# Optimization experiments

Measured on AMD Instinct MI355X. Metric: run time of the kernel, lower is better.

## Reference

```python
import jax, jax.numpy as jnp
import numpy as np

N = 262144   # cohort size (k_n)
M = 8192     # number of ordinal anchor indices (len(Hj))


def setup_inputs() -> dict:
    key = jax.random.key(0)
    k1, k2, k3, k4, k5 = jax.random.split(key, 5)
    time = jax.random.uniform(k1, (N,), dtype=jnp.float32) * 1000.0
    event = (jax.random.uniform(k2, (N,), dtype=jnp.float32) < 0.3).astype(jnp.float32)
    y_true0 = jnp.stack([time, event], axis=1)          # [N,2] (time, event)
    y_true1 = y_true0                                    # second head labels (unused by loss)
    y_pred0 = jax.random.normal(k3, (N, 1), dtype=jnp.float32) * 0.1  # xbeta head 0
    y_pred1 = jax.random.normal(k4, (N, 1), dtype=jnp.float32) * 0.1  # xbeta head 1
    Hj = jnp.sort(jax.random.randint(k5, (M,), 0, N, dtype=jnp.int32))  # static event indices into sorted order
    log_vars = jnp.zeros((2, 1), dtype=jnp.float32)      # layer weights log_var0, log_var1
    return {"y_true0": y_true0, "y_true1": y_true1, "y_pred0": y_pred0,
            "y_pred1": y_pred1, "Hj": Hj, "log_vars": log_vars}


def reference(y_true0, y_true1, y_pred0, y_pred1, Hj, log_vars):
    n = y_true0.shape[0]
    # top_k with k = n == full descending sort by time
    _, order = jax.lax.top_k(y_true0[:, 0], n)

    # ---- neg_log_pl (Cox negative partial log-likelihood, per-sample vector) ----
    xbeta = y_pred0[order, 0]                 # [N] sorted by descending time
    event = y_true0[order, 1]                 # [N]
    denom = jnp.cumsum(jnp.exp(xbeta))        # risk-set cumulative sum
    lossA = -(event * (xbeta - jnp.log(denom)))  # [N]

    # ---- ordinal_loss0 (pairwise ranking over event indices Hj in sorted order) ----
    # intended math: for each j, for ii >= j: cost += 1 - exp(xbeta[Hj[j]] - xbeta[Hj[ii]])
    xb = y_pred1[order, 0]                    # [N] sorted
    xh = xb[Hj]                               # [M]
    m = Hj.shape[0]
    rec = 1.0 - jnp.exp(xh[:, None] - xh[None, :])   # [M,M] rec[j,ii]
    mask = jnp.triu(jnp.ones((m, m), dtype=bool))    # ii >= j
    cost2 = jnp.sum(jnp.where(mask, rec, 0.0))

    # ---- multi_loss combination with learned log variances ----
    lv0 = log_vars[0, 0]
    lv1 = log_vars[1, 0]
    precision1 = jnp.clip(jnp.exp(-lv1), 0.0, 1.0)
    loss = jnp.sum(lossA + lv0) + (precision1 * cost2 + lv1)
    return loss


if __name__ == "__main__":
    out = reference(**setup_inputs())
    print(out)
```

## Files before the change

kernel.cpp:

```cpp
#include <hip/hip_runtime.h>
#include <math.h>


#define BSHIFT 12
#define NBUCK (1 << 19)
#define NREP 4
#define BLK 256
#define NC1 32

#define STORE_U32(p, v) __hip_atomic_store((p), (v), __ATOMIC_RELAXED, __HIP_MEMORY_SCOPE_AGENT)
#define STORE_F32(p, v) __hip_atomic_store((p), (v), __ATOMIC_RELAXED, __HIP_MEMORY_SCOPE_AGENT)
#define STORE_U64(p, v) __hip_atomic_store((unsigned long long*)(p), (v), __ATOMIC_RELAXED, __HIP_MEMORY_SCOPE_AGENT)

template <int GRID>
__device__ __forceinline__ void gbar(unsigned* bar, unsigned gv) {
  __syncthreads();
  if (threadIdx.x == 0) {
    constexpr unsigned BPC = GRID / NC1;
    const unsigned grp = blockIdx.x & (NC1 - 1);
    unsigned a = __hip_atomic_fetch_add(bar + grp * 16, 1u,
                                        __ATOMIC_RELAXED, __HIP_MEMORY_SCOPE_AGENT);
    if (a == gv * BPC - 1u) {
      unsigned b = __hip_atomic_fetch_add(bar + 512, 1u,
                                          __ATOMIC_RELAXED, __HIP_MEMORY_SCOPE_AGENT);
      if (b == gv * NC1 - 1u) {
        #pragma unroll
        for (int i = 0; i < NC1; ++i)
          STORE_U32(bar + 544 + i * 16, gv);
      }
    }
    int guard = 0;
    while (__hip_atomic_load(bar + 544 + grp * 16, __ATOMIC_RELAXED,
                             __HIP_MEMORY_SCOPE_AGENT) < gv) {
      __builtin_amdgcn_s_sleep(8);
      if (++guard > 8000000) break;
    }
  }
  __syncthreads();
}

template <int GRID>
__global__ void __launch_bounds__(BLK, 4)
k_fused(const float2* __restrict__ yt0, const float* __restrict__ yp0,
        const float* __restrict__ yp1, const int* __restrict__ Hj,
        const float* __restrict__ lv, int n, int m,
        unsigned* __restrict__ bar,
        unsigned* __restrict__ count, unsigned* __restrict__ E,
        unsigned* __restrict__ bTot, uint2* __restrict__ skey2,
        unsigned* __restrict__ sidx, float* __restrict__ preS,
        float* __restrict__ seTot, float* __restrict__ xh,
        double* __restrict__ accum, float* __restrict__ out)
{
  constexpr int TOT = GRID * BLK;
  constexpr int BPB = NBUCK / GRID;
  constexpr int BPT = BPB / BLK;
  const int t = threadIdx.x;
  const int g = blockIdx.x;
  const int gtid = g * BLK + t;

  __shared__ unsigned su[BLK];
  __shared__ float    sf[BLK];
  __shared__ float    pb[512];
  __shared__ double   sd[BLK];
  __shared__ float    wt[4];

  const int r = g & (NREP - 1);
  unsigned keyR[2]; float seR[2]; unsigned seqR[2]; unsigned evR[2];
  #pragma unroll
  for (int el = 0; el < 2; ++el) {
    int i = gtid + el * TOT;
    keyR[el] = 0u; seR[el] = 0.f; seqR[el] = 0u; evR[el] = 0u;
    if (i < n) {
      float2 te = yt0[i];
      unsigned key = __float_as_uint(te.x);
      keyR[el] = key;
      evR[el] = (te.y != 0.f) ? 0x80000000u : 0u;
      seR[el] = expf(yp0[i]);
      seqR[el] = atomicAdd(&count[(size_t)(key >> BSHIFT) * NREP + r], 1u);
    }
  }
  gbar<GRID>(bar, 1);

  unsigned incl[BPT]; unsigned thrBase;
  {
    unsigned run = 0u;
    #pragma unroll
    for (int k = 0; k < BPT; ++k) {
      int b = g * BPB + t * BPT + k;
      uint4 c = ((const uint4*)count)[b];
      run += c.x + c.y + c.z + c.w;
      incl[k] = run;
    }
    su[t] = run;
    __syncthreads();
    for (int off2 = 1; off2 < BLK; off2 <<= 1) {
      unsigned v = (t >= off2) ? su[t - off2] : 0u;
      __syncthreads();
      su[t] += v;
      __syncthreads();
    }
    thrBase = (t > 0) ? su[t - 1] : 0u;
    if (t == BLK - 1) STORE_U32(&bTot[g], su[t]);
  }
  gbar<GRID>(bar, 2);

  {
    unsigned part = 0u;
    for (int j = t; j < g; j += BLK) part += bTot[j];
    su[t] = part;
    __syncthreads();
    for (int s = BLK / 2; s > 0; s >>= 1) { if (t < s) su[t] += su[t + s]; __syncthreads(); }
    unsigned bBase = su[0];
    __syncthreads();
    unsigned e0 = bBase + thrBase;
    int ebase = g * BPB + t * BPT;
    if constexpr (BPT == 2) {
      unsigned long long w = ((unsigned long long)(e0 + incl[0]) << 32) | e0;
      STORE_U64(&E[ebase], w);
    } else {
      unsigned long long w0 = ((unsigned long long)(e0 + incl[0]) << 32) | e0;
      unsigned long long w1 = ((unsigned long long)(e0 + incl[2]) << 32) | (e0 + incl[1]);
      STORE_U64(&E[ebase], w0);
      STORE_U64(&E[ebase + 2], w1);
    }
  }
  gbar<GRID>(bar, 3);

  #pragma unroll
  for (int el = 0; el < 2; ++el) {
    int i = gtid + el * TOT;
    if (i < n) {
      unsigned key = keyR[el];
      unsigned b = key >> BSHIFT;
      uint4 c = ((const uint4*)count)[b];
      unsigned cnt = c.x + c.y + c.z + c.w;
      unsigned offr = 0u;
      if (r > 0) offr += c.x;
      if (r > 1) offr += c.y;
      if (r > 2) offr += c.z;
      unsigned start = (unsigned)n - E[b] - cnt;
      unsigned pos = start + offr + seqR[el];
      unsigned long long v =
          ((unsigned long long)__float_as_uint(seR[el]) << 32) | key;
      STORE_U64(&skey2[pos], v);
      STORE_U32(&sidx[pos], (unsigned)i | evR[el]);
    }
  }
  gbar<GRID>(bar, 4);

  if (g < 512) {
    int base = g * (2 * BLK);
    int p0 = base + 2 * t, p1 = p0 + 1;
    float e0 = (p0 < n) ? __uint_as_float(skey2[p0].y) : 0.f;
    float e1 = (p1 < n) ? __uint_as_float(skey2[p1].y) : 0.f;
    float pairv = e0 + e1;
    sf[t] = pairv;
    __syncthreads();
    for (int off2 = 1; off2 < BLK; off2 <<= 1) {
      float v = (t >= off2) ? sf[t - off2] : 0.f;
      __syncthreads();
      sf[t] += v;
      __syncthreads();
    }
    float ex = sf[t] - pairv;
    if (p0 < n) STORE_F32(&preS[p0], ex + e0);
    if (p1 < n) STORE_F32(&preS[p1], ex + e0 + e1);
    if (t == BLK - 1) STORE_F32(&seTot[g], sf[t]);
  }
  gbar<GRID>(bar, 5);

  {
    float a0 = seTot[2 * t];
    float a1 = seTot[2 * t + 1];
    float pairv = a0 + a1;
    sf[t] = pairv;
    __syncthreads();
    for (int off2 = 1; off2 < BLK; off2 <<= 1) {
      float v = (t >= off2) ? sf[t - off2] : 0.f;
      __syncthreads();
      sf[t] += v;
      __syncthreads();
    }
    pb[2 * t]     = sf[t] - a1;
    pb[2 * t + 1] = sf[t];
    __syncthreads();

    double contrib = 0.0;
    #pragma unroll
    for (int el = 0; el < 2; ++el) {
      int p = gtid + el * TOT;
      if (p >= n) continue;
      uint2 kv = skey2[p];
      unsigned key = kv.x;
      float e = __uint_as_float(kv.y);
      unsigned sidv = sidx[p];
      unsigned idx = sidv & 0x7FFFFFFFu;
      bool evb = (sidv >> 31) != 0u;
      unsigned b = key >> BSHIFT;
      uint4 c4 = ((const uint4*)count)[b];
      unsigned cnt = c4.x + c4.y + c4.z + c4.w;
      unsigned end = (unsigned)n - E[b];
      unsigned start = end - cnt;
      if (end > (unsigned)n) end = (unsigned)n;
      if (start > end) start = end;
      float wsum = 0.f;
      unsigned wcnt = 0u;
      unsigned q = start;
      while (q + 8 <= end) {
        uint2 v[8];
        #pragma unroll
        for (int k = 0; k < 8; ++k) v[k] = skey2[q + k];
        #pragma unroll
        for (int k = 0; k < 8; ++k) {
          if (v[k].x > key) { wsum += __uint_as_float(v[k].y); wcnt++; }
          else if (v[k].x == key && (sidx[q + k] & 0x7FFFFFFFu) < idx) {
            wsum += __uint_as_float(v[k].y); wcnt++;
          }
        }
        q += 8;
      }
      for (; q < end; ++q) {
        uint2 v = skey2[q];
        if (v.x > key) { wsum += __uint_as_float(v.y); wcnt++; }
        else if (v.x == key && (sidx[q] & 0x7FFFFFFFu) < idx) {
          wsum += __uint_as_float(v.y); wcnt++;
        }
      }
      unsigned sb = start >> 9;
      float cross = ((sb > 0) ? pb[sb - 1] : 0.f)
                  + ((start & 511u) ? preS[start - 1] : 0.f);
      float denom = cross + wsum + e;
      int rank = (int)(start + wcnt);
      if (evb) contrib += (double)logf(denom / e);
      int lo = 0, hi = m;
      while (lo < hi) { int mid = (lo + hi) >> 1; if (Hj[mid] < rank) lo = mid + 1; else hi = mid; }
      if (lo < m && Hj[lo] == rank) {
        float xb1 = yp1[idx];
        for (int j = lo; j < m && Hj[j] == rank; ++j) STORE_F32(&xh[j], xb1);
      }
    }
    sd[t] = contrib;
    __syncthreads();
    for (int s = 128; s > 0; s >>= 1) { if (t < s) sd[t] += sd[t + s]; __syncthreads(); }
    if (t == 0) atomicAdd(accum, sd[0]);
  }
  gbar<GRID>(bar, 6);

  if (g != 0) return;
  {
    int lane = t & 63;
    int w = t >> 6;
    double acc = 0.0;
    float carry = 0.f;
    int passes = (m + 2047) / 2048;
    for (int pss = passes - 1; pss >= 0; --pss) {
      int base = pss * 2048 + t * 8;
      float x[8], eb[8];
      float c = 0.f;
      #pragma unroll
      for (int k = 0; k < 8; ++k) {
        int j = base + k;
        x[k] = (j < m) ? xh[j] : 0.f;
        eb[k] = (j < m) ? expf(-x[k]) : 0.f;
        c += eb[k];
      }
      float s = c;
      #pragma unroll
      for (int d = 1; d < 64; d <<= 1) {
        float o = __shfl_down(s, d, 64);
        if (lane + d < 64) s += o;
      }
      float wtot = __shfl(s, 0, 64);
      if (lane == 0) wt[w] = wtot;
      __syncthreads();
      float after = 0.f, ptot = 0.f;
      #pragma unroll
      for (int w2 = 0; w2 < 4; ++w2) { ptot += wt[w2]; if (w2 > w) after += wt[w2]; }
      float S = (s - c) + after + carry;
      #pragma unroll
      for (int k = 7; k >= 0; --k) {
        int j = base + k;
        S += eb[k];
        if (j < m) acc += (double)(expf(x[k]) * S);
      }
      __syncthreads();
      carry += ptot;
    }
    sd[t] = acc;
    __syncthreads();
    for (int s2 = 128; s2 > 0; s2 >>= 1) { if (t < s2) sd[t] += sd[t + s2]; __syncthreads(); }
    if (t == 0) {
      double T = (double)m * (double)(m + 1) * 0.5;
      double cost2 = T - sd[0];
      float lv0 = lv[0], lv1 = lv[1];
      float prec1 = fminf(expf(-lv1), 1.0f);
      double loss = *accum + (double)n * (double)lv0 + (double)prec1 * cost2 + (double)lv1;
      out[0] = (float)loss;
    }
  }
}

extern "C" void kernel_launch(void* const* d_in, const int* in_sizes, int n_in,
                              void* d_out, int out_size, void* d_ws, size_t ws_size,
                              hipStream_t stream) {
  (void)n_in; (void)out_size;
  const float2* yt0 = (const float2*)d_in[0];
  const float*  yp0 = (const float*)d_in[2];
  const float*  yp1 = (const float*)d_in[3];
  const int*    Hj  = (const int*)d_in[4];
  const float*  lv  = (const float*)d_in[5];
  int n = in_sizes[0] / 2;
  int m = in_sizes[4];

  char* ws = (char*)d_ws;
  unsigned* bar   = (unsigned*)ws;
  double*   accum = (double*)(ws + 6144);
  size_t off = 8192;
  auto alloc = [&](size_t bytes) -> void* {
    void* p = ws + off;
    off += (bytes + 255) & ~(size_t)255;
    return p;
  };
  unsigned* count = (unsigned*)alloc((size_t)NBUCK * NREP * 4);
  unsigned* E     = (unsigned*)alloc((size_t)NBUCK * 4);
  unsigned* bTot  = (unsigned*)alloc(1024 * 4);
  uint2*    skey2 = (uint2*)alloc((size_t)n * 8);
  unsigned* sidx  = (unsigned*)alloc((size_t)n * 4);
  float*    preS  = (float*)alloc((size_t)n * 4);
  float*    seTot = (float*)alloc(1024 * 4);
  float*    xh    = (float*)alloc((size_t)m * 4);
  if (off > ws_size) return;

  hipMemsetAsync(ws, 0, 8192 + (size_t)NBUCK * NREP * 4, stream);

  k_fused<1024><<<dim3(1024), dim3(BLK), 0, stream>>>(
      yt0, yp0, yp1, Hj, lv, n, m, bar, count, E, bTot, skey2, sidx,
      preS, seTot, xh, accum, (float*)d_out);
}
```

Measured before the change: 138.1 us.

## Fold per-bucket exp sums into histogram atomics and drop the global prefix-scan stages

```diff
diff --git a/kernel.cpp b/kernel.cpp
--- a/kernel.cpp
+++ b/kernel.cpp
@@ -4,9 +4,9 @@
 
 #define BSHIFT 12
 #define NBUCK (1 << 19)
-#define NREP 4
 #define BLK 256
 #define NC1 32
+#define M40 ((1ull << 40) - 1)
 
 #define STORE_U32(p, v) __hip_atomic_store((p), (v), __ATOMIC_RELAXED, __HIP_MEMORY_SCOPE_AGENT)
 #define STORE_F32(p, v) __hip_atomic_store((p), (v), __ATOMIC_RELAXED, __HIP_MEMORY_SCOPE_AGENT)
@@ -32,8 +32,8 @@
     int guard = 0;
     while (__hip_atomic_load(bar + 544 + grp * 16, __ATOMIC_RELAXED,
                              __HIP_MEMORY_SCOPE_AGENT) < gv) {
-      __builtin_amdgcn_s_sleep(8);
-      if (++guard > 8000000) break;
+      __builtin_amdgcn_s_sleep(1);
+      if (++guard > 2000000) break;
     }
   }
   __syncthreads();
@@ -45,10 +45,10 @@
         const float* __restrict__ yp1, const int* __restrict__ Hj,
         const float* __restrict__ lv, int n, int m,
         unsigned* __restrict__ bar,
-        unsigned* __restrict__ count, unsigned* __restrict__ E,
-        unsigned* __restrict__ bTot, uint2* __restrict__ skey2,
-        unsigned* __restrict__ sidx, float* __restrict__ preS,
-        float* __restrict__ seTot, float* __restrict__ xh,
+        unsigned long long* __restrict__ rec, unsigned* __restrict__ bitmap,
+        uint4* __restrict__ Epack, unsigned* __restrict__ bTot,
+        float* __restrict__ fTot, uint2* __restrict__ skey2,
+        unsigned* __restrict__ sidx, float* __restrict__ xh,
         double* __restrict__ accum, float* __restrict__ out)
 {
   constexpr int TOT = GRID * BLK;
@@ -59,12 +59,10 @@
   const int gtid = g * BLK + t;
 
   __shared__ unsigned su[BLK];
-  __shared__ float    sf[BLK];
-  __shared__ float    pb[512];
+  __shared__ float    sff[BLK];
   __shared__ double   sd[BLK];
   __shared__ float    wt[4];
 
-  const int r = g & (NREP - 1);
   unsigned keyR[2]; float seR[2]; unsigned seqR[2]; unsigned evR[2];
   #pragma unroll
   for (int el = 0; el < 2; ++el) {
@@ -75,53 +73,70 @@
       unsigned key = __float_as_uint(te.x);
       keyR[el] = key;
       evR[el] = (te.y != 0.f) ? 0x80000000u : 0u;
-      seR[el] = expf(yp0[i]);
-      seqR[el] = atomicAdd(&count[(size_t)(key >> BSHIFT) * NREP + r], 1u);
-    }
+      float e = expf(yp0[i]);
+      seR[el] = e;
+      unsigned long long qe = (unsigned long long)(e * 16777216.0f + 0.5f);
+      if (qe > (1ull << 32)) qe = (1ull << 32);
+      unsigned long long ret =
+          atomicAdd(&rec[key >> BSHIFT], (1ull << 40) | qe);
+      seqR[el] = (unsigned)(ret >> 40);
+    }
+  }
+  for (int j = gtid; j < m; j += TOT) {
+    int h = Hj[j];
+    atomicOr(&bitmap[h >> 5], 1u << (h & 31));
   }
   gbar<GRID>(bar, 1);
 
-  unsigned incl[BPT]; unsigned thrBase;
+  unsigned cK[BPT]; float fK[BPT];
+  unsigned thrC; float thrF;
   {
-    unsigned run = 0u;
+    unsigned runc = 0u; float runf = 0.f;
     #pragma unroll
     for (int k = 0; k < BPT; ++k) {
-      int b = g * BPB + t * BPT + k;
-      uint4 c = ((const uint4*)count)[b];
-      run += c.x + c.y + c.z + c.w;
-      incl[k] = run;
-    }
-    su[t] = run;
+      int b = NBUCK - 1 - (g * BPB + t * BPT + k);
+      unsigned long long v = rec[b];
+      cK[k] = (unsigned)(v >> 40);
+      fK[k] = (float)((double)(v & M40) * (1.0 / 16777216.0));
+      runc += cK[k]; runf += fK[k];
+    }
+    su[t] = runc; sff[t] = runf;
     __syncthreads();
     for (int off2 = 1; off2 < BLK; off2 <<= 1) {
-      unsigned v = (t >= off2) ? su[t - off2] : 0u;
-      __syncthreads();
-      su[t] += v;
-      __syncthreads();
-    }
-    thrBase = (t > 0) ? su[t - 1] : 0u;
-    if (t == BLK - 1) STORE_U32(&bTot[g], su[t]);
+      unsigned uc = (t >= off2) ? su[t - off2] : 0u;
+      float    uf = (t >= off2) ? sff[t - off2] : 0.f;
+      __syncthreads();
+      su[t] += uc; sff[t] += uf;
+      __syncthreads();
+    }
+    thrC = (t > 0) ? su[t - 1] : 0u;
+    thrF = (t > 0) ? sff[t - 1] : 0.f;
+    if (t == BLK - 1) { STORE_U32(&bTot[g], su[t]); STORE_F32(&fTot[g], sff[t]); }
   }
   gbar<GRID>(bar, 2);
 
   {
-    unsigned part = 0u;
-    for (int j = t; j < g; j += BLK) part += bTot[j];
-    su[t] = part;
-    __syncthreads();
-    for (int s = BLK / 2; s > 0; s >>= 1) { if (t < s) su[t] += su[t + s]; __syncthreads(); }
-    unsigned bBase = su[0];
-    __syncthreads();
-    unsigned e0 = bBase + thrBase;
-    int ebase = g * BPB + t * BPT;
-    if constexpr (BPT == 2) {
-      unsigned long long w = ((unsigned long long)(e0 + incl[0]) << 32) | e0;
-      STORE_U64(&E[ebase], w);
-    } else {
-      unsigned long long w0 = ((unsigned long long)(e0 + incl[0]) << 32) | e0;
-      unsigned long long w1 = ((unsigned long long)(e0 + incl[2]) << 32) | (e0 + incl[1]);
-      STORE_U64(&E[ebase], w0);
-      STORE_U64(&E[ebase + 2], w1);
+    unsigned partC = 0u; float partF = 0.f;
+    for (int j = t; j < g; j += BLK) { partC += bTot[j]; partF += fTot[j]; }
+    su[t] = partC; sff[t] = partF;
+    __syncthreads();
+    for (int s = BLK / 2; s > 0; s >>= 1) {
+      if (t < s) { su[t] += su[t + s]; sff[t] += sff[t + s]; }
+      __syncthreads();
+    }
+    unsigned baseC = su[0]; float baseF = sff[0];
+    __syncthreads();
+    unsigned preC = 0u; float preF = 0.f;
+    #pragma unroll
+    for (int k = 0; k < BPT; ++k) {
+      int b = NBUCK - 1 - (g * BPB + t * BPT + k);
+      unsigned sfxC = baseC + thrC + preC;
+      float    sfxF = baseF + thrF + preF;
+      unsigned long long w =
+          ((unsigned long long)__float_as_uint(sfxF) << 32) | sfxC;
+      STORE_U64(&Epack[b].x, w);
+      STORE_U32(&Epack[b].z, cK[k]);
+      preC += cK[k]; preF += fK[k];
     }
   }
   gbar<GRID>(bar, 3);
@@ -132,14 +147,8 @@
     if (i < n) {
       unsigned key = keyR[el];
       unsigned b = key >> BSHIFT;
-      uint4 c = ((const uint4*)count)[b];
-      unsigned cnt = c.x + c.y + c.z + c.w;
-      unsigned offr = 0u;
-      if (r > 0) offr += c.x;
-      if (r > 1) offr += c.y;
-      if (r > 2) offr += c.z;
-      unsigned start = (unsigned)n - E[b] - cnt;
-      unsigned pos = start + offr + seqR[el];
+      unsigned start = Epack[b].x;
+      unsigned pos = start + seqR[el];
       unsigned long long v =
           ((unsigned long long)__float_as_uint(seR[el]) << 32) | key;
       STORE_U64(&skey2[pos], v);
@@ -148,59 +157,21 @@
   }
   gbar<GRID>(bar, 4);
 
-  if (g < 512) {
-    int base = g * (2 * BLK);
-    int p0 = base + 2 * t, p1 = p0 + 1;
-    float e0 = (p0 < n) ? __uint_as_float(skey2[p0].y) : 0.f;
-    float e1 = (p1 < n) ? __uint_as_float(skey2[p1].y) : 0.f;
-    float pairv = e0 + e1;
-    sf[t] = pairv;
-    __syncthreads();
-    for (int off2 = 1; off2 < BLK; off2 <<= 1) {
-      float v = (t >= off2) ? sf[t - off2] : 0.f;
-      __syncthreads();
-      sf[t] += v;
-      __syncthreads();
-    }
-    float ex = sf[t] - pairv;
-    if (p0 < n) STORE_F32(&preS[p0], ex + e0);
-    if (p1 < n) STORE_F32(&preS[p1], ex + e0 + e1);
-    if (t == BLK - 1) STORE_F32(&seTot[g], sf[t]);
-  }
-  gbar<GRID>(bar, 5);
-
   {
-    float a0 = seTot[2 * t];
-    float a1 = seTot[2 * t + 1];
-    float pairv = a0 + a1;
-    sf[t] = pairv;
-    __syncthreads();
-    for (int off2 = 1; off2 < BLK; off2 <<= 1) {
-      float v = (t >= off2) ? sf[t - off2] : 0.f;
-      __syncthreads();
-      sf[t] += v;
-      __syncthreads();
-    }
-    pb[2 * t]     = sf[t] - a1;
-    pb[2 * t + 1] = sf[t];
-    __syncthreads();
-
     double contrib = 0.0;
     #pragma unroll
     for (int el = 0; el < 2; ++el) {
-      int p = gtid + el * TOT;
-      if (p >= n) continue;
-      uint2 kv = skey2[p];
-      unsigned key = kv.x;
-      float e = __uint_as_float(kv.y);
-      unsigned sidv = sidx[p];
-      unsigned idx = sidv & 0x7FFFFFFFu;
-      bool evb = (sidv >> 31) != 0u;
+      int i = gtid + el * TOT;
+      if (i >= n) continue;
+      unsigned key = keyR[el];
+      float e = seR[el];
+      unsigned idx = (unsigned)i;
+      bool evb = evR[el] != 0u;
       unsigned b = key >> BSHIFT;
-      uint4 c4 = ((const uint4*)count)[b];
-      unsigned cnt = c4.x + c4.y + c4.z + c4.w;
-      unsigned end = (unsigned)n - E[b];
-      unsigned start = end - cnt;
+      uint4 ep = Epack[b];
+      unsigned start = ep.x;
+      float cross = __uint_as_float(ep.y);
+      unsigned end = start + ep.z;
       if (end > (unsigned)n) end = (unsigned)n;
       if (start > end) start = end;
       float wsum = 0.f;
@@ -226,17 +197,16 @@
           wsum += __uint_as_float(v.y); wcnt++;
         }
       }
-      unsigned sb = start >> 9;
-      float cross = ((sb > 0) ? pb[sb - 1] : 0.f)
-                  + ((start & 511u) ? preS[start - 1] : 0.f);
       float denom = cross + wsum + e;
       int rank = (int)(start + wcnt);
       if (evb) contrib += (double)logf(denom / e);
-      int lo = 0, hi = m;
-      while (lo < hi) { int mid = (lo + hi) >> 1; if (Hj[mid] < rank) lo = mid + 1; else hi = mid; }
-      if (lo < m && Hj[lo] == rank) {
-        float xb1 = yp1[idx];
-        for (int j = lo; j < m && Hj[j] == rank; ++j) STORE_F32(&xh[j], xb1);
+      if ((bitmap[rank >> 5] >> (rank & 31)) & 1u) {
+        int lo = 0, hi = m;
+        while (lo < hi) { int mid = (lo + hi) >> 1; if (Hj[mid] < rank) lo = mid + 1; else hi = mid; }
+        if (lo < m && Hj[lo] == rank) {
+          float xb1 = yp1[idx];
+          for (int j = lo; j < m && Hj[j] == rank; ++j) STORE_F32(&xh[j], xb1);
+        }
       }
     }
     sd[t] = contrib;
@@ -244,7 +214,7 @@
     for (int s = 128; s > 0; s >>= 1) { if (t < s) sd[t] += sd[t + s]; __syncthreads(); }
     if (t == 0) atomicAdd(accum, sd[0]);
   }
-  gbar<GRID>(bar, 6);
+  gbar<GRID>(bar, 5);
 
   if (g != 0) return;
   {
@@ -321,19 +291,36 @@
     off += (bytes + 255) & ~(size_t)255;
     return p;
   };
-  unsigned* count = (unsigned*)alloc((size_t)NBUCK * NREP * 4);
-  unsigned* E     = (unsigned*)alloc((size_t)NBUCK * 4);
+  size_t nbm = ((size_t)(n + 31) / 32) * 4;
+  unsigned* bitmap = (unsigned*)alloc(nbm);
+  unsigned long long* rec = (unsigned long long*)alloc((size_t)NBUCK * 8);
+  size_t zbytes = off;
+  uint4*    Epack = (uint4*)alloc((size_t)NBUCK * 16);
   unsigned* bTot  = (unsigned*)alloc(1024 * 4);
+  float*    fTot  = (float*)alloc(1024 * 4);
   uint2*    skey2 = (uint2*)alloc((size_t)n * 8);
   unsigned* sidx  = (unsigned*)alloc((size_t)n * 4);
-  float*    preS  = (float*)alloc((size_t)n * 4);
-  float*    seTot = (float*)alloc(1024 * 4);
   float*    xh    = (float*)alloc((size_t)m * 4);
   if (off > ws_size) return;
 
-  hipMemsetAsync(ws, 0, 8192 + (size_t)NBUCK * NREP * 4, stream);
-
-  k_fused<1024><<<dim3(1024), dim3(BLK), 0, stream>>>(
-      yt0, yp0, yp1, Hj, lv, n, m, bar, count, E, bTot, skey2, sidx,
-      preS, seTot, xh, accum, (float*)d_out);
+  hipMemsetAsync(ws, 0, zbytes, stream);
+
+  static int gridChoice = 0;
+  if (gridChoice == 0) {
+    int nb = 0;
+    hipError_t e1 = hipOccupancyMaxActiveBlocksPerMultiprocessor(&nb, k_fused<1024>, BLK, 0);
+    int dev = 0; hipGetDevice(&dev);
+    hipDeviceProp_t prop;
+    hipError_t e2 = hipGetDeviceProperties(&prop, dev);
+    gridChoice = (e1 == hipSuccess && e2 == hipSuccess &&
+                  nb * prop.multiProcessorCount >= 1024) ? 1024 : 512;
+  }
+  if (gridChoice == 1024)
+    k_fused<1024><<<dim3(1024), dim3(BLK), 0, stream>>>(
+        yt0, yp0, yp1, Hj, lv, n, m, bar, rec, bitmap, Epack, bTot, fTot,
+        skey2, sidx, xh, accum, (float*)d_out);
+  else
+    k_fused<512><<<dim3(512), dim3(BLK), 0, stream>>>(
+        yt0, yp0, yp1, Hj, lv, n, m, bar, rec, bitmap, Epack, bTot, fTot,
+        skey2, sidx, xh, accum, (float*)d_out);
 }
```

New measurement: 155.3 us. 1.12x slower.
